# Kernel tuning notes

Measured on AMD Instinct MI355X. Metric: run time of the kernel, lower is better.

## Reference

```python
import jax, jax.numpy as jnp
from jax import lax
import numpy as np

DC = 3.79
HSTEP = 0.1
EPS = 1e-5
BIG = 1e10

def conv1(x, K):
    p = (K.shape[-1] - 1) // 2
    return lax.conv_general_dilated(x, K, (1,), [(p, p)], dimension_numbers=("NCH", "OIH", "NCH"))

def conv1T(x, K):
    # conv_transpose1d(stride=1, padding=p) == conv1d with flipped kernel and swapped in/out channels
    return conv1(x, jnp.flip(jnp.swapaxes(K, 0, 1), -1))

def masked_instance_norm(x, mask, eps=EPS):
    denom = jnp.sum(mask, axis=2, keepdims=True)
    mean = jnp.sum(x * mask, axis=2, keepdims=True) / denom
    meanm = mean * mask  # original multiplies the broadcast mean by the mask
    var = jnp.sum(((x - meanm) * mask) ** 2, axis=2, keepdims=True) / denom
    return (x - meanm) / jnp.sqrt(var + eps)

def avg_pool3s2(x):
    # torch avg_pool1d(kernel=3, stride=2, padding=1, count_include_pad=True)
    s = lax.reduce_window(x, 0.0, lax.add, (1, 1, 3), (1, 1, 2), [(0, 0), (0, 0), (1, 1)])
    return s / 3.0

def dist_constraint(X, M_fixed, M_padding, dc=DC):
    # X: [nb,3,n]; M_fixed, M_padding: [nb,1,n]. Vectorized (scan) version of the
    # original per-segment python loops: left/right propagation from fixed anchors
    # via unit-step (length dc) cumulative sums, blended by distance weights.
    dX = X[:, :, 1:] - X[:, :, :-1]
    d = jnp.sum(dX * dX, axis=1, keepdims=True)  # [nb,1,n-1]
    avM = jnp.floor((M_padding[..., 1:] + M_padding[..., :-1]) / 2.0) < 0.5
    dXn = dX / jnp.sqrt(d + avM) * jnp.where(avM, 0.0, dc)  # [nb,3,n-1]
    fixed = M_fixed[:, 0, :] == 1  # [nb,n]

    Xt = jnp.moveaxis(X, 2, 0)      # [n,nb,3]
    dXnt = jnp.moveaxis(dXn, 2, 0)  # [n-1,nb,3]
    ft = fixed.T                    # [n,nb]

    def lstep(carry, inp):
        prev, seen, wl = carry
        xj, dxn, fj = inp
        val = jnp.where(fj[:, None] | ~seen[:, None], xj, prev + dxn)
        wl2 = (wl + 1.0) * (~fj)
        return (val, seen | fj, wl2), (val, wl2)

    wl0 = jnp.where(ft[0], 0.0, BIG)
    _, (lv, lw) = lax.scan(lstep, (Xt[0], ft[0], wl0), (Xt[1:], dXnt, ft[1:]))
    Xleft = jnp.concatenate([X[:, :, :1], jnp.moveaxis(lv, 0, 2)], axis=2)
    wl = jnp.concatenate([wl0[:, None], lw.T], axis=1)  # [nb,n]

    def rstep(carry, inp):
        nxt, seen, wr = carry
        xj, dxn, fj = inp
        val = jnp.where(fj[:, None] | ~seen[:, None], xj, nxt - dxn)
        wr2 = (wr + 1.0) * (~fj)
        return (val, seen | fj, wr2), (val, wr2)

    wrN = jnp.where(ft[-1], 0.0, BIG)
    _, (rv, rw) = lax.scan(rstep, (Xt[-1], ft[-1], wrN), (Xt[:-1], dXnt, ft[:-1]), reverse=True)
    Xright = jnp.concatenate([jnp.moveaxis(rv, 0, 2), X[:, :, -1:]], axis=2)
    wr = jnp.concatenate([rw.T, wrN[:, None]], axis=1)

    ws = wl + wr
    ws_safe = jnp.where(ws == 0.0, 1.0, ws)
    cl = jnp.where(ws == 0.0, 0.5, wr / ws_safe)  # weight on Xleft = (wsum-wl)/wsum
    cr = jnp.where(ws == 0.0, 0.5, wl / ws_safe)
    X2 = Xleft * cl[:, None, :] + Xright * cr[:, None, :]
    return X2 * M_padding

def tr2dist(Y):
    # pairwise Euclidean distances from coords [nb,3,n] -> [nb,n,n]
    Z = jnp.swapaxes(Y, 1, 2)
    Z = Z - jnp.mean(Z, axis=1, keepdims=True)
    sq = jnp.sum(Z * Z, axis=2)
    D2 = sq[:, :, None] + sq[:, None, :] - 2.0 * jnp.einsum("bic,bjc->bij", Z, Z)
    return jnp.sqrt(jnp.maximum(D2, 0.0) + 1e-8)

def vnet_forward(x, mask, Ks, W):
    coords = x[:, -4:-1, :]
    mask_coords = jnp.repeat((x[:, -1, :] == 1)[:, None, :], 3, axis=1)
    m = mask[:, None, :]
    nL = len(Ks)
    xc = jax.nn.relu(masked_instance_norm(conv1(x, Ks[0]) * m, m))  # dropout_p=0 -> identity
    xS, mS = [], []
    for i in range(1, nL):
        K = Ks[i]
        if K.shape[0] == K.shape[1]:
            z = jax.nn.relu(masked_instance_norm(conv1(xc, K) * m, m))
            xc = xc - HSTEP * (conv1T(z, K) * m)
        else:
            xS.append(xc)
            xc = jax.nn.relu(masked_instance_norm(conv1(xc, K) * m, m))
            mS.append(m)
            m = (avg_pool3s2(m) >= 0.5).astype(x.dtype)
            xc = avg_pool3s2(xc) * m
    ns = len(xS)
    for i in reversed(range(1, nL)):
        K = Ks[i]
        if K.shape[0] == K.shape[1]:
            z = jax.nn.relu(masked_instance_norm(conv1T(xc, K) * m, m))
            xc = xc - HSTEP * (conv1(z, K) * m)
        else:
            ns -= 1
            m = mS[ns]
            xc = jnp.repeat(xc, 2, axis=-1) * m  # F.interpolate(scale=2, mode='nearest')
            z = masked_instance_norm(conv1T(xc, K) * m, m)
            xc = jax.nn.relu(z) + xS[ns]
    xc = conv1(xc, W) * m
    xc = jnp.where(mask_coords, coords, xc)
    xout = dist_constraint(xc, mask_coords[:, :1, :].astype(x.dtype), m)
    return tr2dist(xout), xout

def setup_inputs() -> dict:
    key = jax.random.key(0)
    ks = jax.random.split(key, 12)
    nb, n = 8, 2048
    feats = jax.random.normal(ks[0], (nb, 20, n), dtype=jnp.float32)
    coords = jax.random.normal(ks[1], (nb, 3, n), dtype=jnp.float32)
    lengths = jax.random.randint(ks[2], (nb,), n // 2, n + 1)
    mask = (jnp.arange(n)[None, :] < lengths[:, None]).astype(jnp.float32)  # ragged padding mask
    flag = (jax.random.uniform(ks[3], (nb, n)) < 0.5).astype(jnp.float32) * mask  # fixed-coord flag
    x = jnp.concatenate([feats, coords, flag[:, None, :]], axis=1)

    def unif(k, shape, stdv):
        return jax.random.uniform(k, shape, jnp.float32, -stdv, stdv)

    K0 = unif(ks[4], (32, 24, 3), 0.1 * 24 / 32)
    K1 = unif(ks[5], (32, 32, 3), 0.01)
    K2 = unif(ks[6], (32, 32, 3), 0.01)
    K3 = unif(ks[7], (64, 32, 3), 0.1 * 32 / 64)
    K4 = unif(ks[8], (64, 64, 3), 0.01)
    K5 = unif(ks[9], (64, 64, 3), 0.01)
    K6 = unif(ks[10], (128, 64, 3), 0.1 * 64 / 128)
    W = 0.1 * jax.random.normal(ks[11], (3, 32, 1), dtype=jnp.float32)
    return {"x": x, "mask": mask, "K0": K0, "K1": K1, "K2": K2, "K3": K3, "K4": K4, "K5": K5, "K6": K6, "W": W}

def reference(x, mask, K0, K1, K2, K3, K4, K5, K6, W):
    dists, xout = vnet_forward(x, mask, [K0, K1, K2, K3, K4, K5, K6], W)
    return (dists, xout)
```

## Files before the change

kernel.cpp:

```cpp
#include <hip/hip_runtime.h>
#include <math.h>

#define HSTEP 0.1f
#define EPS_IN 1e-5f
#define BIGF 1e10f
#define DCF 3.79f

__device__ inline float block_sum1(float v, float* sred) {
    #pragma unroll
    for (int off = 32; off > 0; off >>= 1) v += __shfl_down(v, off);
    int wid = threadIdx.x >> 6;
    int nw  = blockDim.x >> 6;
    if ((threadIdx.x & 63) == 0) sred[wid] = v;
    __syncthreads();
    float total = 0.f;
    for (int i = 0; i < nw; ++i) total += sred[i];
    __syncthreads();
    return total;
}

__device__ inline float2 block_sum2(float a, float b, float2* sred) {
    #pragma unroll
    for (int off = 32; off > 0; off >>= 1) {
        a += __shfl_down(a, off);
        b += __shfl_down(b, off);
    }
    int wid = threadIdx.x >> 6;
    int nw  = blockDim.x >> 6;
    if ((threadIdx.x & 63) == 0) sred[wid] = make_float2(a, b);
    __syncthreads();
    float ta = 0.f, tb = 0.f;
    for (int i = 0; i < nw; ++i) { ta += sred[i].x; tb += sred[i].y; }
    __syncthreads();
    return make_float2(ta, tb);
}

template<int CIN, bool TR>
__global__ void __launch_bounds__(1024)
conv_in_relu_kernel(const float* __restrict__ xin, float* __restrict__ out,
                    const float* __restrict__ K, int Cout, int N,
                    const float* __restrict__ mask, const float* __restrict__ denom,
                    const float* __restrict__ skip)
{
    __shared__ float srow[2048];
    __shared__ float swt[CIN * 3];
    __shared__ float2 sred[16];

    const int b   = blockIdx.x / Cout;
    const int co  = blockIdx.x % Cout;
    const int tid = threadIdx.x;

    for (int i = tid; i < CIN * 3; i += blockDim.x) {
        int ci = i / 3, k = i % 3;
        swt[i] = TR ? K[((size_t)ci * Cout + co) * 3 + (2 - k)]
                    : K[((size_t)co * CIN + ci) * 3 + k];
    }
    __syncthreads();

    const float* mrow = mask + (size_t)b * N;
    const float* xb   = xin + (size_t)b * CIN * N;
    float lsum = 0.f, lss = 0.f;
    for (int n = tid; n < N; n += 1024) {
        float acc = 0.f;
        const float* xr = xb + n;
        #pragma unroll 8
        for (int ci = 0; ci < CIN; ++ci, xr += N) {
            float xm = (n > 0)     ? xr[-1] : 0.f;
            float x0 = xr[0];
            float xp = (n < N - 1) ? xr[1]  : 0.f;
            acc = fmaf(swt[ci * 3 + 0], xm, acc);
            acc = fmaf(swt[ci * 3 + 1], x0, acc);
            acc = fmaf(swt[ci * 3 + 2], xp, acc);
        }
        float v = acc * mrow[n];
        srow[n] = v;
        lsum += v;
        lss  += v * v;
    }
    float dn = denom[b];
    float2 s = block_sum2(lsum, lss, sred);
    float mean = s.x / dn;
    float var  = s.y / dn - mean * mean;
    float inv  = 1.f / sqrtf(var + EPS_IN);

    float* orow = out + ((size_t)b * Cout + co) * N;
    const float* skrow = skip ? skip + ((size_t)b * Cout + co) * N : nullptr;
    for (int n = tid; n < N; n += 1024) {
        float mk = mrow[n];
        float zv = (srow[n] - mean * mk) * inv;
        float r  = fmaxf(zv, 0.f);
        if (skrow) r += skrow[n];
        orow[n] = r;
    }
}

template<int CIN, bool TR>
__global__ void __launch_bounds__(1024)
conv_axpy_kernel(const float* __restrict__ z, float* __restrict__ xc,
                 const float* __restrict__ K, int Cout, int N,
                 const float* __restrict__ mask)
{
    __shared__ float swt[CIN * 3];
    const int b   = blockIdx.x / Cout;
    const int co  = blockIdx.x % Cout;
    const int tid = threadIdx.x;

    for (int i = tid; i < CIN * 3; i += blockDim.x) {
        int ci = i / 3, k = i % 3;
        swt[i] = TR ? K[((size_t)ci * Cout + co) * 3 + (2 - k)]
                    : K[((size_t)co * CIN + ci) * 3 + k];
    }
    __syncthreads();

    const float* mrow = mask + (size_t)b * N;
    const float* zb   = z + (size_t)b * CIN * N;
    float* orow = xc + ((size_t)b * Cout + co) * N;
    for (int n = tid; n < N; n += 1024) {
        float acc = 0.f;
        const float* zr = zb + n;
        #pragma unroll 8
        for (int ci = 0; ci < CIN; ++ci, zr += N) {
            float xm = (n > 0)     ? zr[-1] : 0.f;
            float x0 = zr[0];
            float xp = (n < N - 1) ? zr[1]  : 0.f;
            acc = fmaf(swt[ci * 3 + 0], xm, acc);
            acc = fmaf(swt[ci * 3 + 1], x0, acc);
            acc = fmaf(swt[ci * 3 + 2], xp, acc);
        }
        orow[n] -= HSTEP * acc * mrow[n];
    }
}

__global__ void __launch_bounds__(256)
mask_prep_kernel(const float* __restrict__ mask, float* __restrict__ M1,
                 float* __restrict__ M2, float* __restrict__ d0, float* __restrict__ d1)
{
    __shared__ float sm1[1024];
    __shared__ float sredf[4];
    int b = blockIdx.x, tid = threadIdx.x;
    const float* mr = mask + (size_t)b * 2048;

    float s0 = 0.f;
    for (int n = tid; n < 2048; n += 256) s0 += mr[n];
    float t0 = block_sum1(s0, sredf);
    if (tid == 0) d0[b] = t0;

    for (int n = tid; n < 1024; n += 256) {
        float s = mr[2 * n];
        if (2 * n - 1 >= 0)   s += mr[2 * n - 1];
        if (2 * n + 1 < 2048) s += mr[2 * n + 1];
        float v = (s * (1.f / 3.f) >= 0.5f) ? 1.f : 0.f;
        sm1[n] = v;
        M1[(size_t)b * 1024 + n] = v;
    }
    __syncthreads();
    float s1 = 0.f;
    for (int n = tid; n < 1024; n += 256) s1 += sm1[n];
    float t1 = block_sum1(s1, sredf);
    if (tid == 0) d1[b] = t1;

    for (int n = tid; n < 512; n += 256) {
        float s = sm1[2 * n];
        if (2 * n - 1 >= 0)   s += sm1[2 * n - 1];
        if (2 * n + 1 < 1024) s += sm1[2 * n + 1];
        M2[(size_t)b * 512 + n] = (s * (1.f / 3.f) >= 0.5f) ? 1.f : 0.f;
    }
}

__global__ void pool_x_kernel(const float* __restrict__ xin, float* __restrict__ xout,
                              const float* __restrict__ mnew, int C, int Nin, int Nout, int B)
{
    int idx = blockIdx.x * blockDim.x + threadIdx.x;
    if (idx >= B * C * Nout) return;
    int n  = idx % Nout;
    int bc = idx / Nout;
    int b  = bc / C;
    const float* r = xin + (size_t)bc * Nin;
    float s = r[2 * n];
    if (2 * n - 1 >= 0)  s += r[2 * n - 1];
    if (2 * n + 1 < Nin) s += r[2 * n + 1];
    xout[idx] = s * (1.f / 3.f) * mnew[(size_t)b * Nout + n];
}

__global__ void upsample_kernel(const float* __restrict__ xin, float* __restrict__ xout,
                                const float* __restrict__ mask, int C, int Nout, int B)
{
    int idx = blockIdx.x * blockDim.x + threadIdx.x;
    if (idx >= B * C * Nout) return;
    int n  = idx % Nout;
    int bc = idx / Nout;
    int b  = bc / C;
    xout[idx] = xin[(size_t)bc * (Nout / 2) + (n >> 1)] * mask[(size_t)b * Nout + n];
}

__global__ void __launch_bounds__(1024)
dc_all_kernel(const float* __restrict__ xc32, const float* __restrict__ x,
              const float* __restrict__ W, const float* __restrict__ mask,
              const float* __restrict__ den, float* __restrict__ xout, int N)
{
    __shared__ float sX[3][2048];
    __shared__ float sD[3][2048];
    __shared__ float sM[2048];
    __shared__ unsigned long long smk[32];
    __shared__ float sW[96];

    const int b = blockIdx.x, tid = threadIdx.x;
    if (tid < 96) sW[tid] = W[tid];
    __syncthreads();

    const float* xb      = xc32 + (size_t)b * 32 * N;
    const float* flagrow = x + ((size_t)b * 24 + 23) * N;

    #pragma unroll
    for (int r = 0; r < 2; ++r) {
        int n = tid + r * 1024;
        float mk = mask[(size_t)b * N + n];
        float fl = flagrow[n];
        float v0 = 0.f, v1 = 0.f, v2 = 0.f;
        #pragma unroll 8
        for (int ci = 0; ci < 32; ++ci) {
            float xv = xb[(size_t)ci * N + n];
            v0 = fmaf(sW[0 * 32 + ci], xv, v0);
            v1 = fmaf(sW[1 * 32 + ci], xv, v1);
            v2 = fmaf(sW[2 * 32 + ci], xv, v2);
        }
        v0 *= mk; v1 *= mk; v2 *= mk;
        bool fixed = (fl == 1.f);
        if (fixed) {
            v0 = x[((size_t)b * 24 + 20) * N + n];
            v1 = x[((size_t)b * 24 + 21) * N + n];
            v2 = x[((size_t)b * 24 + 22) * N + n];
        }
        sX[0][n] = v0; sX[1][n] = v1; sX[2][n] = v2; sM[n] = mk;
        unsigned long long bm = __ballot(fixed);
        if ((tid & 63) == 0) smk[n >> 6] = bm;
    }
    __syncthreads();

    #pragma unroll
    for (int r = 0; r < 2; ++r) {
        int n = tid + r * 1024;
        if (n < N - 1) {
            float d0 = sX[0][n + 1] - sX[0][n];
            float d1 = sX[1][n + 1] - sX[1][n];
            float d2 = sX[2][n + 1] - sX[2][n];
            float d  = d0 * d0 + d1 * d1 + d2 * d2;
            bool avM = floorf((sM[n] + sM[n + 1]) * 0.5f) < 0.5f;
            if (avM) {
                sD[0][n] = 0.f; sD[1][n] = 0.f; sD[2][n] = 0.f;
            } else {
                float sq = sqrtf(d);
                sD[0][n] = (d0 / sq) * DCF;
                sD[1][n] = (d1 / sq) * DCF;
                sD[2][n] = (d2 / sq) * DCF;
            }
        }
    }
    __syncthreads();

    int len = (int)den[b];

    #pragma unroll
    for (int r = 0; r < 2; ++r) {
        int j  = tid + r * 1024;
        int cc = j >> 6, jl = j & 63;

        unsigned long long below = smk[cc] & (~0ull >> (63 - jl));
        int p = -1;
        if (below) p = (cc << 6) + 63 - __clzll(below);
        else {
            for (int c2 = cc - 1; c2 >= 0; --c2) {
                unsigned long long m = smk[c2];
                if (m) { p = (c2 << 6) + 63 - __clzll(m); break; }
            }
        }
        float l0, l1, l2, wl;
        if (p >= 0) {
            wl = (float)(j - p);
            l0 = sX[0][p]; l1 = sX[1][p]; l2 = sX[2][p];
            int kend = min(j, len - 1);
            for (int k = p; k < kend; ++k) {
                l0 += sD[0][k]; l1 += sD[1][k]; l2 += sD[2][k];
            }
        } else { wl = BIGF; l0 = sX[0][j]; l1 = sX[1][j]; l2 = sX[2][j]; }

        unsigned long long above = smk[cc] & (~0ull << jl);
        int q = -1;
        if (above) q = (cc << 6) + __ffsll((unsigned long long)above) - 1;
        else {
            for (int c2 = cc + 1; c2 < 32; ++c2) {
                unsigned long long m = smk[c2];
                if (m) { q = (c2 << 6) + __ffsll((unsigned long long)m) - 1; break; }
            }
        }
        float r0, r1, r2, wr;
        if (q >= 0) {
            wr = (float)(q - j);
            r0 = sX[0][q]; r1 = sX[1][q]; r2 = sX[2][q];
            for (int k = q - 1; k >= j; --k) {
                r0 -= sD[0][k]; r1 -= sD[1][k]; r2 -= sD[2][k];
            }
        } else { wr = BIGF; r0 = sX[0][j]; r1 = sX[1][j]; r2 = sX[2][j]; }

        float ws_ = wl + wr;
        float cl, cr;
        if (ws_ == 0.f) { cl = 0.5f; cr = 0.5f; }
        else            { cl = wr / ws_; cr = wl / ws_; }
        float mk = sM[j];
        xout[((size_t)b * 3 + 0) * N + j] = (l0 * cl + r0 * cr) * mk;
        xout[((size_t)b * 3 + 1) * N + j] = (l1 * cl + r1 * cr) * mk;
        xout[((size_t)b * 3 + 2) * N + j] = (l2 * cl + r2 * cr) * mk;
    }
}

__global__ void __launch_bounds__(256)
tr2dist_kernel(const float* __restrict__ Y, float* __restrict__ out, int B, int N)
{
    int i = blockIdx.x % N;
    int b = blockIdx.x / N;
    const float* yb = Y + (size_t)b * 3 * N;
    float y0 = yb[i], y1 = yb[N + i], y2 = yb[2 * N + i];
    float* orow = out + ((size_t)b * N + i) * N;
    for (int j = threadIdx.x; j < N; j += blockDim.x) {
        float d0 = y0 - yb[j];
        float d1 = y1 - yb[N + j];
        float d2 = y2 - yb[2 * N + j];
        orow[j] = sqrtf(fmaf(d0, d0, fmaf(d1, d1, d2 * d2)) + 1e-8f);
    }
}

extern "C" void kernel_launch(void* const* d_in, const int* in_sizes, int n_in,
                              void* d_out, int out_size, void* d_ws, size_t ws_size,
                              hipStream_t stream)
{
    const float* x    = (const float*)d_in[0];
    const float* mask = (const float*)d_in[1];
    const float* K0   = (const float*)d_in[2];
    const float* K1   = (const float*)d_in[3];
    const float* K2   = (const float*)d_in[4];
    const float* K3   = (const float*)d_in[5];
    const float* K4   = (const float*)d_in[6];
    const float* K5   = (const float*)d_in[7];
    const float* K6   = (const float*)d_in[8];
    const float* W    = (const float*)d_in[9];
    float* out = (float*)d_out;
    float* ws  = (float*)d_ws;

    const int B = 8, N = 2048;
    size_t off = 0;
    auto alloc = [&](size_t nf) { float* p = ws + off; off += nf; return p; };

    float* M1   = alloc((size_t)B * 1024);
    float* M2   = alloc((size_t)B * 512);
    float* DEN0 = alloc(8);
    float* DEN1 = alloc(8);
    float* BUF0 = alloc(1048576);
    float* BUF1 = alloc(1048576);
    float* BUF2 = alloc(1048576);
    float* BUF3 = alloc(1048576);
    (void)ws_size; (void)in_sizes; (void)n_in; (void)out_size;

    auto cdiv = [](int a, int b_) { return (a + b_ - 1) / b_; };
    float* XOUT = out + (size_t)B * N * N;

    mask_prep_kernel<<<8, 256, 0, stream>>>(mask, M1, M2, DEN0, DEN1);

    conv_in_relu_kernel<24, false><<<B * 32, 1024, 0, stream>>>(x, BUF0, K0, 32, 2048, mask, DEN0, nullptr);

    conv_in_relu_kernel<32, false><<<B * 32, 1024, 0, stream>>>(BUF0, BUF1, K1, 32, 2048, mask, DEN0, nullptr);
    conv_axpy_kernel<32, true><<<B * 32, 1024, 0, stream>>>(BUF1, BUF0, K1, 32, 2048, mask);
    conv_in_relu_kernel<32, false><<<B * 32, 1024, 0, stream>>>(BUF0, BUF1, K2, 32, 2048, mask, DEN0, nullptr);
    conv_axpy_kernel<32, true><<<B * 32, 1024, 0, stream>>>(BUF1, BUF0, K2, 32, 2048, mask);

    conv_in_relu_kernel<32, false><<<B * 64, 1024, 0, stream>>>(BUF0, BUF1, K3, 64, 2048, mask, DEN0, nullptr);
    pool_x_kernel<<<cdiv(B * 64 * 1024, 256), 256, 0, stream>>>(BUF1, BUF2, M1, 64, 2048, 1024, B);

    conv_in_relu_kernel<64, false><<<B * 64, 1024, 0, stream>>>(BUF2, BUF1, K4, 64, 1024, M1, DEN1, nullptr);
    conv_axpy_kernel<64, true><<<B * 64, 1024, 0, stream>>>(BUF1, BUF2, K4, 64, 1024, M1);
    conv_in_relu_kernel<64, false><<<B * 64, 1024, 0, stream>>>(BUF2, BUF1, K5, 64, 1024, M1, DEN1, nullptr);
    conv_axpy_kernel<64, true><<<B * 64, 1024, 0, stream>>>(BUF1, BUF2, K5, 64, 1024, M1);

    conv_in_relu_kernel<64, false><<<B * 128, 1024, 0, stream>>>(BUF2, BUF1, K6, 128, 1024, M1, DEN1, nullptr);
    pool_x_kernel<<<cdiv(B * 128 * 512, 256), 256, 0, stream>>>(BUF1, BUF3, M2, 128, 1024, 512, B);

    upsample_kernel<<<cdiv(B * 128 * 1024, 256), 256, 0, stream>>>(BUF3, BUF1, M1, 128, 1024, B);
    conv_in_relu_kernel<128, true><<<B * 64, 1024, 0, stream>>>(BUF1, BUF3, K6, 64, 1024, M1, DEN1, BUF2);

    conv_in_relu_kernel<64, true><<<B * 64, 1024, 0, stream>>>(BUF3, BUF1, K5, 64, 1024, M1, DEN1, nullptr);
    conv_axpy_kernel<64, false><<<B * 64, 1024, 0, stream>>>(BUF1, BUF3, K5, 64, 1024, M1);
    conv_in_relu_kernel<64, true><<<B * 64, 1024, 0, stream>>>(BUF3, BUF1, K4, 64, 1024, M1, DEN1, nullptr);
    conv_axpy_kernel<64, false><<<B * 64, 1024, 0, stream>>>(BUF1, BUF3, K4, 64, 1024, M1);

    upsample_kernel<<<cdiv(B * 64 * 2048, 256), 256, 0, stream>>>(BUF3, BUF1, mask, 64, 2048, B);
    conv_in_relu_kernel<64, true><<<B * 32, 1024, 0, stream>>>(BUF1, BUF2, K3, 32, 2048, mask, DEN0, BUF0);

    conv_in_relu_kernel<32, true><<<B * 32, 1024, 0, stream>>>(BUF2, BUF1, K2, 32, 2048, mask, DEN0, nullptr);
    conv_axpy_kernel<32, false><<<B * 32, 1024, 0, stream>>>(BUF1, BUF2, K2, 32, 2048, mask);
    conv_in_relu_kernel<32, true><<<B * 32, 1024, 0, stream>>>(BUF2, BUF1, K1, 32, 2048, mask, DEN0, nullptr);
    conv_axpy_kernel<32, false><<<B * 32, 1024, 0, stream>>>(BUF1, BUF2, K1, 32, 2048, mask);

    dc_all_kernel<<<B, 1024, 0, stream>>>(BUF2, x, W, mask, DEN0, XOUT, N);

    tr2dist_kernel<<<B * N, 256, 0, stream>>>(XOUT, out, B, N);
}
```

Baseline: 422.4 us.

## Unify conv kernels with fused pool/upsample and tile the pairwise distance kernel

Replaces the separate conv+instance-norm and conv-axpy kernels with one templated kernel. It computes four outputs per thread using float4 loads, fuses the avg-pool into the preceding conv and the nearest upsample into the following conv, and packs two output channels per block at length 1024. The pairwise-distance kernel now loads the coordinates into shared memory once per block, processes 32 rows per block, and writes float4s instead of launching one block per row. This removes several full-tensor round trips and many launches. It hardcodes sizes (N=2048, 8 batches) and relies on aligned vector access.

New measurement: 589.3 us. 1.4x slower.

```diff
diff --git a/kernel.cpp b/kernel.cpp
--- a/kernel.cpp
+++ b/kernel.cpp
@@ -6,6 +6,122 @@
 #define BIGF 1e10f
 #define DCF 3.79f
 
+template<int CIN, int NS, bool UPS, bool AXPY>
+__global__ void __launch_bounds__(512)
+conv_k(const float* __restrict__ in, float* __restrict__ out,
+       const float* __restrict__ Kw, int Cout, int TR,
+       const float* __restrict__ mask, const float* __restrict__ den_g,
+       const float* __restrict__ skip, float* __restrict__ pool,
+       const float* __restrict__ mhalf)
+{
+    constexpr int T = (NS == 2048) ? 512 : 256;
+    constexpr int P = (NS == 2048) ? 1 : 2;
+    __shared__ float swt_s[P * CIN * 3];
+    __shared__ float s_red[32];
+    __shared__ __align__(16) float s_row[2048];
+
+    const int tid  = threadIdx.x;
+    const int grp  = (P == 2) ? (tid >> 8) : 0;
+    const int tsub = (P == 2) ? (tid & 255) : tid;
+    const int cpb  = Cout / P;
+    const int b    = blockIdx.x / cpb;
+    const int co   = (blockIdx.x % cpb) * P + grp;
+    float* swt = swt_s + grp * CIN * 3;
+
+    for (int i = tsub; i < CIN * 3; i += T) {
+        int ci = i / 3, k = i % 3;
+        swt[i] = TR ? Kw[((size_t)ci * Cout + co) * 3 + (2 - k)]
+                    : Kw[((size_t)co * CIN + ci) * 3 + k];
+    }
+    __syncthreads();
+
+    const int srcw = UPS ? (NS >> 1) : NS;
+    const float* in_b = in + (size_t)b * CIN * srcw;
+    const float* mrow = mask + (size_t)b * NS;
+
+    const int n0 = tsub * 4;
+    const float4 mv = *(const float4*)(mrow + n0);
+    float a0 = 0.f, a1 = 0.f, a2 = 0.f, a3 = 0.f;
+    #pragma unroll 4
+    for (int ci = 0; ci < CIN; ++ci) {
+        const float* src = in_b + (size_t)ci * srcw;
+        float xl, x0, x1, x2, x3, xr;
+        if (!UPS) {
+            const float4 v = *(const float4*)(src + n0);
+            x0 = v.x; x1 = v.y; x2 = v.z; x3 = v.w;
+            xl = (n0 > 0)      ? src[n0 - 1] : 0.f;
+            xr = (n0 + 4 < NS) ? src[n0 + 4] : 0.f;
+        } else {
+            const float2 s = *(const float2*)(src + (n0 >> 1));
+            x0 = s.x * mv.x; x1 = s.x * mv.y;
+            x2 = s.y * mv.z; x3 = s.y * mv.w;
+            xl = (n0 > 0)      ? src[(n0 - 1) >> 1] * mrow[n0 - 1] : 0.f;
+            xr = (n0 + 4 < NS) ? src[(n0 + 4) >> 1] * mrow[n0 + 4] : 0.f;
+        }
+        const float w0 = swt[ci * 3], w1 = swt[ci * 3 + 1], w2 = swt[ci * 3 + 2];
+        a0 = fmaf(w0, xl, fmaf(w1, x0, fmaf(w2, x1, a0)));
+        a1 = fmaf(w0, x0, fmaf(w1, x1, fmaf(w2, x2, a1)));
+        a2 = fmaf(w0, x1, fmaf(w1, x2, fmaf(w2, x3, a2)));
+        a3 = fmaf(w0, x2, fmaf(w1, x3, fmaf(w2, xr, a3)));
+    }
+    const float v0 = a0 * mv.x, v1 = a1 * mv.y, v2 = a2 * mv.z, v3 = a3 * mv.w;
+    float* orow = out ? out + ((size_t)b * Cout + co) * NS + n0 : nullptr;
+
+    if constexpr (AXPY) {
+        float4 cur = *(const float4*)orow;
+        float4 rr;
+        rr.x = cur.x - HSTEP * v0; rr.y = cur.y - HSTEP * v1;
+        rr.z = cur.z - HSTEP * v2; rr.w = cur.w - HSTEP * v3;
+        *(float4*)orow = rr;
+    } else {
+        float ls = v0 + v1 + v2 + v3;
+        float lq = v0 * v0 + v1 * v1 + v2 * v2 + v3 * v3;
+        #pragma unroll
+        for (int off = 32; off > 0; off >>= 1) {
+            ls += __shfl_down(ls, off);
+            lq += __shfl_down(lq, off);
+        }
+        const int wig = tsub >> 6;
+        const int wpg = T >> 6;
+        if ((tsub & 63) == 0) { s_red[grp * 16 + wig * 2] = ls; s_red[grp * 16 + wig * 2 + 1] = lq; }
+        __syncthreads();
+        float ts = 0.f, tq = 0.f;
+        for (int i2 = 0; i2 < wpg; ++i2) { ts += s_red[grp * 16 + i2 * 2]; tq += s_red[grp * 16 + i2 * 2 + 1]; }
+        const float den  = den_g[b];
+        const float mean = ts / den;
+        const float inv  = 1.f / sqrtf(tq / den - mean * mean + EPS_IN);
+        float r0 = fmaxf((v0 - mean * mv.x) * inv, 0.f);
+        float r1 = fmaxf((v1 - mean * mv.y) * inv, 0.f);
+        float r2 = fmaxf((v2 - mean * mv.z) * inv, 0.f);
+        float r3 = fmaxf((v3 - mean * mv.w) * inv, 0.f);
+        if (skip) {
+            const float4 sk = *(const float4*)(skip + ((size_t)b * Cout + co) * NS + n0);
+            r0 += sk.x; r1 += sk.y; r2 += sk.z; r3 += sk.w;
+        }
+        if (orow) {
+            float4 rr; rr.x = r0; rr.y = r1; rr.z = r2; rr.w = r3;
+            *(float4*)orow = rr;
+        }
+        if (pool) {
+            float* srow = s_row + grp * NS;
+            srow[n0] = r0; srow[n0 + 1] = r1; srow[n0 + 2] = r2; srow[n0 + 3] = r3;
+            __syncthreads();
+            const int Nh = NS >> 1;
+            if (tsub < (T >> 1)) {
+                const int np0 = tsub * 4;
+                const float4 mh = *(const float4*)(mhalf + (size_t)b * Nh + np0);
+                float zm1 = (np0 > 0) ? srow[2 * np0 - 1] : 0.f;
+                float4 p;
+                p.x = (zm1 + srow[2*np0] + srow[2*np0+1]) * (1.f/3.f) * mh.x;
+                p.y = (srow[2*np0+1] + srow[2*np0+2] + srow[2*np0+3]) * (1.f/3.f) * mh.y;
+                p.z = (srow[2*np0+3] + srow[2*np0+4] + srow[2*np0+5]) * (1.f/3.f) * mh.z;
+                p.w = (srow[2*np0+5] + srow[2*np0+6] + srow[2*np0+7]) * (1.f/3.f) * mh.w;
+                *(float4*)(pool + ((size_t)b * Cout + co) * Nh + np0) = p;
+            }
+        }
+    }
+}
+
 __device__ inline float block_sum1(float v, float* sred) {
     #pragma unroll
     for (int off = 32; off > 0; off >>= 1) v += __shfl_down(v, off);
@@ -17,118 +133,6 @@
     for (int i = 0; i < nw; ++i) total += sred[i];
     __syncthreads();
     return total;
-}
-
-__device__ inline float2 block_sum2(float a, float b, float2* sred) {
-    #pragma unroll
-    for (int off = 32; off > 0; off >>= 1) {
-        a += __shfl_down(a, off);
-        b += __shfl_down(b, off);
-    }
-    int wid = threadIdx.x >> 6;
-    int nw  = blockDim.x >> 6;
-    if ((threadIdx.x & 63) == 0) sred[wid] = make_float2(a, b);
-    __syncthreads();
-    float ta = 0.f, tb = 0.f;
-    for (int i = 0; i < nw; ++i) { ta += sred[i].x; tb += sred[i].y; }
-    __syncthreads();
-    return make_float2(ta, tb);
-}
-
-template<int CIN, bool TR>
-__global__ void __launch_bounds__(1024)
-conv_in_relu_kernel(const float* __restrict__ xin, float* __restrict__ out,
-                    const float* __restrict__ K, int Cout, int N,
-                    const float* __restrict__ mask, const float* __restrict__ denom,
-                    const float* __restrict__ skip)
-{
-    __shared__ float srow[2048];
-    __shared__ float swt[CIN * 3];
-    __shared__ float2 sred[16];
-
-    const int b   = blockIdx.x / Cout;
-    const int co  = blockIdx.x % Cout;
-    const int tid = threadIdx.x;
-
-    for (int i = tid; i < CIN * 3; i += blockDim.x) {
-        int ci = i / 3, k = i % 3;
-        swt[i] = TR ? K[((size_t)ci * Cout + co) * 3 + (2 - k)]
-                    : K[((size_t)co * CIN + ci) * 3 + k];
-    }
-    __syncthreads();
-
-    const float* mrow = mask + (size_t)b * N;
-    const float* xb   = xin + (size_t)b * CIN * N;
-    float lsum = 0.f, lss = 0.f;
-    for (int n = tid; n < N; n += 1024) {
-        float acc = 0.f;
-        const float* xr = xb + n;
-        #pragma unroll 8
-        for (int ci = 0; ci < CIN; ++ci, xr += N) {
-            float xm = (n > 0)     ? xr[-1] : 0.f;
-            float x0 = xr[0];
-            float xp = (n < N - 1) ? xr[1]  : 0.f;
-            acc = fmaf(swt[ci * 3 + 0], xm, acc);
-            acc = fmaf(swt[ci * 3 + 1], x0, acc);
-            acc = fmaf(swt[ci * 3 + 2], xp, acc);
-        }
-        float v = acc * mrow[n];
-        srow[n] = v;
-        lsum += v;
-        lss  += v * v;
-    }
-    float dn = denom[b];
-    float2 s = block_sum2(lsum, lss, sred);
-    float mean = s.x / dn;
-    float var  = s.y / dn - mean * mean;
-    float inv  = 1.f / sqrtf(var + EPS_IN);
-
-    float* orow = out + ((size_t)b * Cout + co) * N;
-    const float* skrow = skip ? skip + ((size_t)b * Cout + co) * N : nullptr;
-    for (int n = tid; n < N; n += 1024) {
-        float mk = mrow[n];
-        float zv = (srow[n] - mean * mk) * inv;
-        float r  = fmaxf(zv, 0.f);
-        if (skrow) r += skrow[n];
-        orow[n] = r;
-    }
-}
-
-template<int CIN, bool TR>
-__global__ void __launch_bounds__(1024)
-conv_axpy_kernel(const float* __restrict__ z, float* __restrict__ xc,
-                 const float* __restrict__ K, int Cout, int N,
-                 const float* __restrict__ mask)
-{
-    __shared__ float swt[CIN * 3];
-    const int b   = blockIdx.x / Cout;
-    const int co  = blockIdx.x % Cout;
-    const int tid = threadIdx.x;
-
-    for (int i = tid; i < CIN * 3; i += blockDim.x) {
-        int ci = i / 3, k = i % 3;
-        swt[i] = TR ? K[((size_t)ci * Cout + co) * 3 + (2 - k)]
-                    : K[((size_t)co * CIN + ci) * 3 + k];
-    }
-    __syncthreads();
-
-    const float* mrow = mask + (size_t)b * N;
-    const float* zb   = z + (size_t)b * CIN * N;
-    float* orow = xc + ((size_t)b * Cout + co) * N;
-    for (int n = tid; n < N; n += 1024) {
-        float acc = 0.f;
-        const float* zr = zb + n;
-        #pragma unroll 8
-        for (int ci = 0; ci < CIN; ++ci, zr += N) {
-            float xm = (n > 0)     ? zr[-1] : 0.f;
-            float x0 = zr[0];
-            float xp = (n < N - 1) ? zr[1]  : 0.f;
-            acc = fmaf(swt[ci * 3 + 0], xm, acc);
-            acc = fmaf(swt[ci * 3 + 1], x0, acc);
-            acc = fmaf(swt[ci * 3 + 2], xp, acc);
-        }
-        orow[n] -= HSTEP * acc * mrow[n];
-    }
 }
 
 __global__ void __launch_bounds__(256)
@@ -165,32 +169,6 @@
         if (2 * n + 1 < 1024) s += sm1[2 * n + 1];
         M2[(size_t)b * 512 + n] = (s * (1.f / 3.f) >= 0.5f) ? 1.f : 0.f;
     }
-}
-
-__global__ void pool_x_kernel(const float* __restrict__ xin, float* __restrict__ xout,
-                              const float* __restrict__ mnew, int C, int Nin, int Nout, int B)
-{
-    int idx = blockIdx.x * blockDim.x + threadIdx.x;
-    if (idx >= B * C * Nout) return;
-    int n  = idx % Nout;
-    int bc = idx / Nout;
-    int b  = bc / C;
-    const float* r = xin + (size_t)bc * Nin;
-    float s = r[2 * n];
-    if (2 * n - 1 >= 0)  s += r[2 * n - 1];
-    if (2 * n + 1 < Nin) s += r[2 * n + 1];
-    xout[idx] = s * (1.f / 3.f) * mnew[(size_t)b * Nout + n];
-}
-
-__global__ void upsample_kernel(const float* __restrict__ xin, float* __restrict__ xout,
-                                const float* __restrict__ mask, int C, int Nout, int B)
-{
-    int idx = blockIdx.x * blockDim.x + threadIdx.x;
-    if (idx >= B * C * Nout) return;
-    int n  = idx % Nout;
-    int bc = idx / Nout;
-    int b  = bc / C;
-    xout[idx] = xin[(size_t)bc * (Nout / 2) + (n >> 1)] * mask[(size_t)b * Nout + n];
 }
 
 __global__ void __launch_bounds__(1024)
@@ -286,11 +264,11 @@
 
         unsigned long long above = smk[cc] & (~0ull << jl);
         int q = -1;
-        if (above) q = (cc << 6) + __ffsll((unsigned long long)above) - 1;
+        if (above) q = (cc << 6) + __ffsll(above) - 1;
         else {
             for (int c2 = cc + 1; c2 < 32; ++c2) {
                 unsigned long long m = smk[c2];
-                if (m) { q = (c2 << 6) + __ffsll((unsigned long long)m) - 1; break; }
+                if (m) { q = (c2 << 6) + __ffsll(m) - 1; break; }
             }
         }
         float r0, r1, r2, wr;
@@ -302,8 +280,7 @@
             }
         } else { wr = BIGF; r0 = sX[0][j]; r1 = sX[1][j]; r2 = sX[2][j]; }
 
-        float ws_ = wl + wr;
-        float cl, cr;
+        float ws_ = wl + wr, cl, cr;
         if (ws_ == 0.f) { cl = 0.5f; cr = 0.5f; }
         else            { cl = wr / ws_; cr = wl / ws_; }
         float mk = sM[j];
@@ -314,18 +291,38 @@
 }
 
 __global__ void __launch_bounds__(256)
-tr2dist_kernel(const float* __restrict__ Y, float* __restrict__ out, int B, int N)
-{
-    int i = blockIdx.x % N;
-    int b = blockIdx.x / N;
-    const float* yb = Y + (size_t)b * 3 * N;
-    float y0 = yb[i], y1 = yb[N + i], y2 = yb[2 * N + i];
-    float* orow = out + ((size_t)b * N + i) * N;
-    for (int j = threadIdx.x; j < N; j += blockDim.x) {
-        float d0 = y0 - yb[j];
-        float d1 = y1 - yb[N + j];
-        float d2 = y2 - yb[2 * N + j];
-        orow[j] = sqrtf(fmaf(d0, d0, fmaf(d1, d1, d2 * d2)) + 1e-8f);
+tr2dist_kernel(const float* __restrict__ Y, float* __restrict__ out, int N)
+{
+    __shared__ __align__(16) float y[6144];
+    const int b    = blockIdx.x >> 6;
+    const int tile = blockIdx.x & 63;
+    const int tid  = threadIdx.x;
+    const float* yb = Y + (size_t)b * 3 * 2048;
+    #pragma unroll
+    for (int k = 0; k < 6; ++k)
+        *(float4*)(y + (tid + k * 256) * 4) = *(const float4*)(yb + (tid + k * 256) * 4);
+    __syncthreads();
+
+    const int j0 = tid * 8;
+    float w0[8], w1[8], w2[8];
+    #pragma unroll
+    for (int k = 0; k < 8; ++k) {
+        w0[k] = y[j0 + k]; w1[k] = y[2048 + j0 + k]; w2[k] = y[4096 + j0 + k];
+    }
+    for (int r = 0; r < 32; ++r) {
+        const int i = tile * 32 + r;
+        const float a0 = y[i], a1 = y[2048 + i], a2 = y[4096 + i];
+        float o[8];
+        #pragma unroll
+        for (int k = 0; k < 8; ++k) {
+            float d0 = a0 - w0[k], d1 = a1 - w1[k], d2 = a2 - w2[k];
+            o[k] = sqrtf(fmaf(d0, d0, fmaf(d1, d1, fmaf(d2, d2, 1e-8f))));
+        }
+        float* orow = out + ((size_t)b * 2048 + i) * 2048 + j0;
+        float4 q0; q0.x = o[0]; q0.y = o[1]; q0.z = o[2]; q0.w = o[3];
+        float4 q1; q1.x = o[4]; q1.y = o[5]; q1.z = o[6]; q1.w = o[7];
+        *(float4*)orow = q0;
+        *(float4*)(orow + 4) = q1;
     }
 }
 
@@ -345,61 +342,49 @@
     const float* W    = (const float*)d_in[9];
     float* out = (float*)d_out;
     float* ws  = (float*)d_ws;
+    (void)in_sizes; (void)n_in; (void)out_size; (void)ws_size;
 
     const int B = 8, N = 2048;
-    size_t off = 0;
-    auto alloc = [&](size_t nf) { float* p = ws + off; off += nf; return p; };
-
-    float* M1   = alloc((size_t)B * 1024);
-    float* M2   = alloc((size_t)B * 512);
-    float* DEN0 = alloc(8);
-    float* DEN1 = alloc(8);
-    float* BUF0 = alloc(1048576);
-    float* BUF1 = alloc(1048576);
-    float* BUF2 = alloc(1048576);
-    float* BUF3 = alloc(1048576);
-    (void)ws_size; (void)in_sizes; (void)n_in; (void)out_size;
-
-    auto cdiv = [](int a, int b_) { return (a + b_ - 1) / b_; };
+    const size_t S = 65536;
+    float* B0 = ws;
+    float* B1 = ws + 8 * S;
+    float* B2 = ws + 16 * S;
+    float* B3 = ws + 24 * S;
+    float* M1   = ws + 32 * S;
+    float* M2   = M1 + 8 * 1024;
+    float* DEN0 = M2 + 8 * 512;
+    float* DEN1 = DEN0 + 8;
     float* XOUT = out + (size_t)B * N * N;
+    const float* NUL = nullptr;
 
     mask_prep_kernel<<<8, 256, 0, stream>>>(mask, M1, M2, DEN0, DEN1);
 
-    conv_in_relu_kernel<24, false><<<B * 32, 1024, 0, stream>>>(x, BUF0, K0, 32, 2048, mask, DEN0, nullptr);
-
-    conv_in_relu_kernel<32, false><<<B * 32, 1024, 0, stream>>>(BUF0, BUF1, K1, 32, 2048, mask, DEN0, nullptr);
-    conv_axpy_kernel<32, true><<<B * 32, 1024, 0, stream>>>(BUF1, BUF0, K1, 32, 2048, mask);
-    conv_in_relu_kernel<32, false><<<B * 32, 1024, 0, stream>>>(BUF0, BUF1, K2, 32, 2048, mask, DEN0, nullptr);
-    conv_axpy_kernel<32, true><<<B * 32, 1024, 0, stream>>>(BUF1, BUF0, K2, 32, 2048, mask);
-
-    conv_in_relu_kernel<32, false><<<B * 64, 1024, 0, stream>>>(BUF0, BUF1, K3, 64, 2048, mask, DEN0, nullptr);
-    pool_x_kernel<<<cdiv(B * 64 * 1024, 256), 256, 0, stream>>>(BUF1, BUF2, M1, 64, 2048, 1024, B);
-
-    conv_in_relu_kernel<64, false><<<B * 64, 1024, 0, stream>>>(BUF2, BUF1, K4, 64, 1024, M1, DEN1, nullptr);
-    conv_axpy_kernel<64, true><<<B * 64, 1024, 0, stream>>>(BUF1, BUF2, K4, 64, 1024, M1);
-    conv_in_relu_kernel<64, false><<<B * 64, 1024, 0, stream>>>(BUF2, BUF1, K5, 64, 1024, M1, DEN1, nullptr);
-    conv_axpy_kernel<64, true><<<B * 64, 1024, 0, stream>>>(BUF1, BUF2, K5, 64, 1024, M1);
-
-    conv_in_relu_kernel<64, false><<<B * 128, 1024, 0, stream>>>(BUF2, BUF1, K6, 128, 1024, M1, DEN1, nullptr);
-    pool_x_kernel<<<cdiv(B * 128 * 512, 256), 256, 0, stream>>>(BUF1, BUF3, M2, 128, 1024, 512, B);
-
-    upsample_kernel<<<cdiv(B * 128 * 1024, 256), 256, 0, stream>>>(BUF3, BUF1, M1, 128, 1024, B);
-    conv_in_relu_kernel<128, true><<<B * 64, 1024, 0, stream>>>(BUF1, BUF3, K6, 64, 1024, M1, DEN1, BUF2);
-
-    conv_in_relu_kernel<64, true><<<B * 64, 1024, 0, stream>>>(BUF3, BUF1, K5, 64, 1024, M1, DEN1, nullptr);
-    conv_axpy_kernel<64, false><<<B * 64, 1024, 0, stream>>>(BUF1, BUF3, K5, 64, 1024, M1);
-    conv_in_relu_kernel<64, true><<<B * 64, 1024, 0, stream>>>(BUF3, BUF1, K4, 64, 1024, M1, DEN1, nullptr);
-    conv_axpy_kernel<64, false><<<B * 64, 1024, 0, stream>>>(BUF1, BUF3, K4, 64, 1024, M1);
-
-    upsample_kernel<<<cdiv(B * 64 * 2048, 256), 256, 0, stream>>>(BUF3, BUF1, mask, 64, 2048, B);
-    conv_in_relu_kernel<64, true><<<B * 32, 1024, 0, stream>>>(BUF1, BUF2, K3, 32, 2048, mask, DEN0, BUF0);
-
-    conv_in_relu_kernel<32, true><<<B * 32, 1024, 0, stream>>>(BUF2, BUF1, K2, 32, 2048, mask, DEN0, nullptr);
-    conv_axpy_kernel<32, false><<<B * 32, 1024, 0, stream>>>(BUF1, BUF2, K2, 32, 2048, mask);
-    conv_in_relu_kernel<32, true><<<B * 32, 1024, 0, stream>>>(BUF2, BUF1, K1, 32, 2048, mask, DEN0, nullptr);
-    conv_axpy_kernel<32, false><<<B * 32, 1024, 0, stream>>>(BUF1, BUF2, K1, 32, 2048, mask);
-
-    dc_all_kernel<<<B, 1024, 0, stream>>>(BUF2, x, W, mask, DEN0, XOUT, N);
-
-    tr2dist_kernel<<<B * N, 256, 0, stream>>>(XOUT, out, B, N);
-}
+    conv_k<24,2048,false,false><<<256, 512, 0, stream>>>(x,  B0, K0, 32, 0, mask, DEN0, NUL, nullptr, NUL);
+    conv_k<32,2048,false,false><<<256, 512, 0, stream>>>(B0, B1, K1, 32, 0, mask, DEN0, NUL, nullptr, NUL);
+    conv_k<32,2048,false,true ><<<256, 512, 0, stream>>>(B1, B0, K1, 32, 1, mask, DEN0, NUL, nullptr, NUL);
+    conv_k<32,2048,false,false><<<256, 512, 0, stream>>>(B0, B1, K2, 32, 0, mask, DEN0, NUL, nullptr, NUL);
+    conv_k<32,2048,false,true ><<<256, 512, 0, stream>>>(B1, B0, K2, 32, 1, mask, DEN0, NUL, nullptr, NUL);
+    conv_k<32,2048,false,false><<<512, 512, 0, stream>>>(B0, nullptr, K3, 64, 0, mask, DEN0, NUL, B2, M1);
+
+    conv_k<64,1024,false,false><<<256, 512, 0, stream>>>(B2, B1, K4, 64, 0, M1, DEN1, NUL, nullptr, NUL);
+    conv_k<64,1024,false,true ><<<256, 512, 0, stream>>>(B1, B2, K4, 64, 1, M1, DEN1, NUL, nullptr, NUL);
+    conv_k<64,1024,false,false><<<256, 512, 0, stream>>>(B2, B1, K5, 64, 0, M1, DEN1, NUL, nullptr, NUL);
+    conv_k<64,1024,false,true ><<<256, 512, 0, stream>>>(B1, B2, K5, 64, 1, M1, DEN1, NUL, nullptr, NUL);
+    conv_k<64,1024,false,false><<<512, 512, 0, stream>>>(B2, nullptr, K6, 128, 0, M1, DEN1, NUL, B3, M2);
+
+    conv_k<128,1024,true ,false><<<256, 512, 0, stream>>>(B3, B1, K6, 64, 1, M1, DEN1, B2, nullptr, NUL);
+    conv_k<64,1024,false,false><<<256, 512, 0, stream>>>(B1, B2, K5, 64, 1, M1, DEN1, NUL, nullptr, NUL);
+    conv_k<64,1024,false,true ><<<256, 512, 0, stream>>>(B2, B1, K5, 64, 0, M1, DEN1, NUL, nullptr, NUL);
+    conv_k<64,1024,false,false><<<256, 512, 0, stream>>>(B1, B2, K4, 64, 1, M1, DEN1, NUL, nullptr, NUL);
+    conv_k<64,1024,false,true ><<<256, 512, 0, stream>>>(B2, B1, K4, 64, 0, M1, DEN1, NUL, nullptr, NUL);
+
+    conv_k<64,2048,true ,false><<<256, 512, 0, stream>>>(B1, B2, K3, 32, 1, mask, DEN0, B0, nullptr, NUL);
+    conv_k<32,2048,false,false><<<256, 512, 0, stream>>>(B2, B1, K2, 32, 1, mask, DEN0, NUL, nullptr, NUL);
+    conv_k<32,2048,false,true ><<<256, 512, 0, stream>>>(B1, B2, K2, 32, 0, mask, DEN0, NUL, nullptr, NUL);
+    conv_k<32,2048,false,false><<<256, 512, 0, stream>>>(B2, B1, K1, 32, 1, mask, DEN0, NUL, nullptr, NUL);
+    conv_k<32,2048,false,true ><<<256, 512, 0, stream>>>(B1, B2, K1, 32, 0, mask, DEN0, NUL, nullptr, NUL);
+
+    dc_all_kernel<<<8, 1024, 0, stream>>>(B2, x, W, mask, DEN0, XOUT, N);
+
+    tr2dist_kernel<<<8 * 64, 256, 0, stream>>>(XOUT, out, N);
+}
```
